# Kernel tuning notes

Measured on AMD Instinct MI355X. Metric: run time of the kernel, lower is better.

Reference implementation:

```python
import jax, jax.numpy as jnp
import numpy as np

H = 2048            # hidden_size
IN = 64             # input_size
EMB = 8             # EMBEDDING_DIMS
LIN = IN - 4 + 4 * EMB  # 92, LSTM input width
NH = 13             # number of prediction heads
MAXO = 9            # max head output width (gear)
HEAD_OUTS = [5, 1, 1, 1, 1, 1, 1, 1, 9, 1, 3, 1, 1]
LN_EPS = 1e-5


def setup_inputs() -> dict:
    key = jax.random.key(0)
    ks = jax.random.split(key, 22)
    s = 1.0 / np.sqrt(H)
    d = {}
    d["lap_cont"] = jax.random.normal(ks[0], (1, 1, IN - 4), jnp.float32)
    d["idx"] = jax.random.randint(ks[1], (1, 1, 4), 0, 5)  # compound, driver, track, team
    d["h_s"] = 0.1 * jax.random.normal(ks[2], (2, 1, H), jnp.float32)
    d["c_s"] = 0.1 * jax.random.normal(ks[3], (2, 1, H), jnp.float32)
    d["emb_team"] = 0.02 * jax.random.normal(ks[4], (10, EMB), jnp.float32)
    d["emb_track"] = 0.02 * jax.random.normal(ks[5], (48, EMB), jnp.float32)
    d["emb_driver"] = 0.02 * jax.random.normal(ks[6], (46, EMB), jnp.float32)
    d["emb_compound"] = 0.02 * jax.random.normal(ks[7], (5, EMB), jnp.float32)
    d["W_ih0"] = s * jax.random.normal(ks[8], (4 * H, LIN), jnp.float32)
    d["W_hh0"] = s * jax.random.normal(ks[9], (4 * H, H), jnp.float32)
    d["b_ih0"] = s * jax.random.normal(ks[10], (4 * H,), jnp.float32)
    d["b_hh0"] = s * jax.random.normal(ks[11], (4 * H,), jnp.float32)
    d["W_ih1"] = s * jax.random.normal(ks[12], (4 * H, H), jnp.float32)
    d["W_hh1"] = s * jax.random.normal(ks[13], (4 * H, H), jnp.float32)
    d["b_ih1"] = s * jax.random.normal(ks[14], (4 * H,), jnp.float32)
    d["b_hh1"] = s * jax.random.normal(ks[15], (4 * H,), jnp.float32)
    d["ln_g"] = jnp.ones((H,), jnp.float32)
    d["ln_b"] = jnp.zeros((H,), jnp.float32)
    d["head_W1"] = 0.02 * jax.random.normal(ks[16], (NH, 64, H), jnp.float32)
    d["head_b1"] = 0.02 * jax.random.normal(ks[17], (NH, 64), jnp.float32)
    d["head_W2"] = 0.02 * jax.random.normal(ks[18], (NH, MAXO, 64), jnp.float32)  # padded to MAXO
    d["head_b2"] = 0.02 * jax.random.normal(ks[19], (NH, MAXO), jnp.float32)
    return d


def _lstm_cell(x, h, c, Wih, Whh, bih, bhh):
    # x:[1,in], h,c:[1,H]; PyTorch gate order i,f,g,o
    g = x @ Wih.T + bih + h @ Whh.T + bhh
    i, f, gg, o = jnp.split(g, 4, axis=-1)
    c_new = jax.nn.sigmoid(f) * c + jax.nn.sigmoid(i) * jnp.tanh(gg)
    h_new = jax.nn.sigmoid(o) * jnp.tanh(c_new)
    return h_new, c_new


def reference(lap_cont, idx, h_s, c_s, emb_team, emb_track, emb_driver, emb_compound,
              W_ih0, W_hh0, b_ih0, b_hh0, W_ih1, W_hh1, b_ih1, b_hh1,
              ln_g, ln_b, head_W1, head_b1, head_W2, head_b2):
    # Embeddings (idx order: compound, driver, track_status, team)
    comp_e = emb_compound[idx[:, :, 0]]
    drv_e = emb_driver[idx[:, :, 1]]
    trk_e = emb_track[idx[:, :, 2]]
    team_e = emb_team[idx[:, :, 3]]
    x = jnp.concatenate([lap_cont, team_e, trk_e, drv_e, comp_e], axis=-1)  # [1,1,LIN]

    x2 = x[0]  # seq_len=1 -> single cell step; [1,LIN]
    h0, c0 = _lstm_cell(x2, h_s[0], c_s[0], W_ih0, W_hh0, b_ih0, b_hh0)
    h1, c1 = _lstm_cell(h0, h_s[1], c_s[1], W_ih1, W_hh1, b_ih1, b_hh1)
    new_h = jnp.stack([h0, h1], axis=0)
    new_c = jnp.stack([c0, c1], axis=0)

    h_t = h1[None]  # [1,1,H]
    mu = jnp.mean(h_t, axis=-1, keepdims=True)
    var = jnp.mean(jnp.square(h_t - mu), axis=-1, keepdims=True)
    h_t = (h_t - mu) * jax.lax.rsqrt(var + LN_EPS) * ln_g + ln_b

    # All 13 heads fused: Dropout is identity at inference
    hid = jax.nn.relu(jnp.einsum('bsh,koh->bsko', h_t, head_W1) + head_b1)  # [1,1,13,64]
    outs = jnp.einsum('bsko,kpo->bskp', hid, head_W2) + head_b2              # [1,1,13,9]

    heads = [outs[:, :, k, :HEAD_OUTS[k]] for k in range(NH)]
    return (new_h, new_c, *heads)
```

## Files before the change

kernel.cpp:

```cpp
#include <hip/hip_runtime.h>

#define H 2048

__device__ __align__(16) float g_p1[4 * H];
__device__ __align__(16) float g_h0[H];
__device__ __align__(16) float g_h1[H];
__device__ __align__(16) float g_hid[13 * 64];

__device__ __forceinline__ float sg(float x) { return 1.f / (1.f + __expf(-x)); }

__device__ __forceinline__ float wred(float x) {
    #pragma unroll
    for (int o = 32; o > 0; o >>= 1) x += __shfl_down(x, o);
    return x;
}

__device__ __forceinline__ float dotg(const float* __restrict__ row,
                                      const float* __restrict__ vec, int lane) {
    float acc = 0.f;
    #pragma unroll
    for (int i = 0; i < 8; i++) {
        int c = i * 256 + lane * 4;
        float4 a = *reinterpret_cast<const float4*>(row + c);
        float4 v = *reinterpret_cast<const float4*>(vec + c);
        acc = fmaf(a.x, v.x, acc); acc = fmaf(a.y, v.y, acc);
        acc = fmaf(a.z, v.z, acc); acc = fmaf(a.w, v.w, acc);
    }
    return acc;
}

__global__ __launch_bounds__(256) void k1(
    const float* __restrict__ lap, const int* __restrict__ idx,
    const float* __restrict__ h_s, const float* __restrict__ c_s,
    const float* __restrict__ e_team, const float* __restrict__ e_trk,
    const float* __restrict__ e_drv, const float* __restrict__ e_cmp,
    const float* __restrict__ Wih0, const float* __restrict__ Whh0,
    const float* __restrict__ bih0, const float* __restrict__ bhh0,
    const float* __restrict__ Whh1, const float* __restrict__ bih1,
    const float* __restrict__ bhh1, float* __restrict__ out)
{
    __shared__ float vec[H];
    __shared__ float xsh[96];
    int tid = threadIdx.x, w = tid >> 6, lane = tid & 63;
    int b = blockIdx.x;
    bool l0 = b < 512;
    const float* src = l0 ? h_s : (h_s + H);
    #pragma unroll
    for (int i = 0; i < 8; i++) vec[tid + i * 256] = src[tid + i * 256];
    if (l0 && tid < 92) {
        float v;
        if (tid < 60)      v = lap[tid];
        else if (tid < 68) v = e_team[idx[3] * 8 + tid - 60];
        else if (tid < 76) v = e_trk [idx[2] * 8 + tid - 68];
        else if (tid < 84) v = e_drv [idx[1] * 8 + tid - 76];
        else               v = e_cmp [idx[0] * 8 + tid - 84];
        xsh[tid] = v;
    }
    __syncthreads();

    if (l0) {
        int j = b * 4 + w;
        float acc[4];
        #pragma unroll
        for (int g = 0; g < 4; g++) {
            long row = j + (long)g * H;
            float a = dotg(Whh0 + row * H, vec, lane);
            const float* wr = Wih0 + row * 92;
            float p = xsh[lane] * wr[lane];
            if (lane < 28) p += xsh[lane + 64] * wr[lane + 64];
            acc[g] = a + p;
        }
        #pragma unroll
        for (int g = 0; g < 4; g++) acc[g] = wred(acc[g]);
        if (lane == 0) {
            float gi = acc[0] + bih0[j]         + bhh0[j];
            float gf = acc[1] + bih0[j + H]     + bhh0[j + H];
            float gg = acc[2] + bih0[j + 2 * H] + bhh0[j + 2 * H];
            float go = acc[3] + bih0[j + 3 * H] + bhh0[j + 3 * H];
            float cp = c_s[j];
            float cn = sg(gf) * cp + sg(gi) * tanhf(gg);
            float hn = sg(go) * tanhf(cn);
            out[j]         = hn;
            out[2 * H + j] = cn;
            g_h0[j] = hn;
        }
    } else {
        int rb = (b - 512) * 16 + w * 4;
        float acc[4];
        #pragma unroll
        for (int r = 0; r < 4; r++) acc[r] = dotg(Whh1 + (long)(rb + r) * H, vec, lane);
        #pragma unroll
        for (int r = 0; r < 4; r++) acc[r] = wred(acc[r]);
        if (lane == 0) {
            #pragma unroll
            for (int r = 0; r < 4; r++) g_p1[rb + r] = acc[r] + bih1[rb + r] + bhh1[rb + r];
        }
    }
}

__global__ __launch_bounds__(256) void k2(
    const float* __restrict__ Wih1, const float* __restrict__ c_s,
    float* __restrict__ out)
{
    __shared__ float vec[H];
    int tid = threadIdx.x, w = tid >> 6, lane = tid & 63;
    #pragma unroll
    for (int i = 0; i < 8; i++) vec[tid + i * 256] = g_h0[tid + i * 256];
    __syncthreads();
    int j = blockIdx.x * 4 + w;
    float acc[4];
    #pragma unroll
    for (int g = 0; g < 4; g++) acc[g] = dotg(Wih1 + (long)(j + g * H) * H, vec, lane);
    #pragma unroll
    for (int g = 0; g < 4; g++) acc[g] = wred(acc[g]);
    if (lane == 0) {
        float gi = acc[0] + g_p1[j];
        float gf = acc[1] + g_p1[j + H];
        float gg = acc[2] + g_p1[j + 2 * H];
        float go = acc[3] + g_p1[j + 3 * H];
        float cp = c_s[H + j];
        float cn = sg(gf) * cp + sg(gi) * tanhf(gg);
        float hn = sg(go) * tanhf(cn);
        out[H + j]     = hn;
        out[3 * H + j] = cn;
        g_h1[j] = hn;
    }
}

__global__ __launch_bounds__(256) void k3(
    const float* __restrict__ ln_g, const float* __restrict__ ln_b,
    const float* __restrict__ W1, const float* __restrict__ b1)
{
    __shared__ float ht[H];
    __shared__ float red[8];
    __shared__ float mvs[2];
    int tid = threadIdx.x, w = tid >> 6, lane = tid & 63;
    float v[8];
    float s = 0.f, s2 = 0.f;
    #pragma unroll
    for (int i = 0; i < 8; i++) {
        float x = g_h1[tid + i * 256];
        v[i] = x; s += x; s2 += x * x;
    }
    s = wred(s); s2 = wred(s2);
    if (lane == 0) { red[w] = s; red[4 + w] = s2; }
    __syncthreads();
    if (tid == 0) {
        float ts = red[0] + red[1] + red[2] + red[3];
        float t2 = red[4] + red[5] + red[6] + red[7];
        float mu = ts / (float)H;
        float var = t2 / (float)H - mu * mu;
        mvs[0] = mu; mvs[1] = rsqrtf(var + 1e-5f);
    }
    __syncthreads();
    float mu = mvs[0], rs = mvs[1];
    #pragma unroll
    for (int i = 0; i < 8; i++) {
        int e = tid + i * 256;
        ht[e] = (v[i] - mu) * rs * ln_g[e] + ln_b[e];
    }
    __syncthreads();
    int k  = blockIdx.x >> 3;
    int u0 = (blockIdx.x & 7) * 8 + w * 2;
    #pragma unroll
    for (int u = 0; u < 2; u++) {
        int o = u0 + u;
        float acc = dotg(W1 + ((long)k * 64 + o) * H, ht, lane);
        acc = wred(acc);
        if (lane == 0) {
            float r = acc + b1[k * 64 + o];
            g_hid[k * 64 + o] = r > 0.f ? r : 0.f;
        }
    }
}

__global__ __launch_bounds__(128) void k4(
    const float* __restrict__ W2, const float* __restrict__ b2,
    float* __restrict__ out)
{
    const int HO[13]  = {5,1,1,1,1,1,1,1,9,1,3,1,1};
    const int OFF[13] = {0,5,6,7,8,9,10,11,12,21,22,25,26};
    int t = threadIdx.x;
    if (t >= 117) return;
    int k = t / 9, p = t % 9;
    if (p >= HO[k]) return;
    const float* wr = W2 + ((long)k * 9 + p) * 64;
    const float* hp = g_hid + k * 64;
    float acc = b2[k * 9 + p];
    #pragma unroll
    for (int o = 0; o < 64; o++) acc = fmaf(hp[o], wr[o], acc);
    out[4 * H + OFF[k] + p] = acc;
}

extern "C" void kernel_launch(void* const* d_in, const int* in_sizes, int n_in,
                              void* d_out, int out_size, void* d_ws, size_t ws_size,
                              hipStream_t stream) {
    const float* lap    = (const float*)d_in[0];
    const int*   idx    = (const int*)  d_in[1];
    const float* h_s    = (const float*)d_in[2];
    const float* c_s    = (const float*)d_in[3];
    const float* e_team = (const float*)d_in[4];
    const float* e_trk  = (const float*)d_in[5];
    const float* e_drv  = (const float*)d_in[6];
    const float* e_cmp  = (const float*)d_in[7];
    const float* Wih0   = (const float*)d_in[8];
    const float* Whh0   = (const float*)d_in[9];
    const float* bih0   = (const float*)d_in[10];
    const float* bhh0   = (const float*)d_in[11];
    const float* Wih1   = (const float*)d_in[12];
    const float* Whh1   = (const float*)d_in[13];
    const float* bih1   = (const float*)d_in[14];
    const float* bhh1   = (const float*)d_in[15];
    const float* ln_g   = (const float*)d_in[16];
    const float* ln_b   = (const float*)d_in[17];
    const float* hW1    = (const float*)d_in[18];
    const float* hb1    = (const float*)d_in[19];
    const float* hW2    = (const float*)d_in[20];
    const float* hb2    = (const float*)d_in[21];
    float* out = (float*)d_out;

    k1<<<1024, 256, 0, stream>>>(lap, idx, h_s, c_s, e_team, e_trk, e_drv, e_cmp,
                                 Wih0, Whh0, bih0, bhh0, Whh1, bih1, bhh1, out);
    k2<<<512, 256, 0, stream>>>(Wih1, c_s, out);
    k3<<<104, 256, 0, stream>>>(ln_g, ln_b, hW1, hb1);
    k4<<<1, 128, 0, stream>>>(hW2, hb2, out);
}
```

Before: 249.8 us.

## Assign one weight row per wave and batch row loads before FMAs

Each wave now computes a single matrix row instead of four, so the GEMV kernels launch four times as many blocks (k3 twice as many). Layer-0 and layer-1 gate combination moves to a shared-memory exchange across the four waves of a block. The dot-product helper issues all eight float4 weight loads up front before the FMA loop, to raise memory-level parallelism. The cost is more blocks that each redundantly stage the hidden vector into LDS, plus an extra block-wide barrier.

```diff
diff --git a/kernel.cpp b/kernel.cpp
--- a/kernel.cpp
+++ b/kernel.cpp
@@ -15,16 +15,18 @@
     return x;
 }
 
-__device__ __forceinline__ float dotg(const float* __restrict__ row,
-                                      const float* __restrict__ vec, int lane) {
+__device__ __forceinline__ float dotrow(const float* __restrict__ row,
+                                        const float* __restrict__ vecLDS, int lane) {
+    float4 a[8];
+    #pragma unroll
+    for (int i = 0; i < 8; i++)
+        a[i] = *reinterpret_cast<const float4*>(row + i * 256 + lane * 4);
     float acc = 0.f;
     #pragma unroll
     for (int i = 0; i < 8; i++) {
-        int c = i * 256 + lane * 4;
-        float4 a = *reinterpret_cast<const float4*>(row + c);
-        float4 v = *reinterpret_cast<const float4*>(vec + c);
-        acc = fmaf(a.x, v.x, acc); acc = fmaf(a.y, v.y, acc);
-        acc = fmaf(a.z, v.z, acc); acc = fmaf(a.w, v.w, acc);
+        float4 v = *reinterpret_cast<const float4*>(vecLDS + i * 256 + lane * 4);
+        acc = fmaf(a[i].x, v.x, acc); acc = fmaf(a[i].y, v.y, acc);
+        acc = fmaf(a[i].z, v.z, acc); acc = fmaf(a[i].w, v.w, acc);
     }
     return acc;
 }
@@ -41,9 +43,10 @@
 {
     __shared__ float vec[H];
     __shared__ float xsh[96];
+    __shared__ float gsh[4];
     int tid = threadIdx.x, w = tid >> 6, lane = tid & 63;
     int b = blockIdx.x;
-    bool l0 = b < 512;
+    bool l0 = b < 2048;
     const float* src = l0 ? h_s : (h_s + H);
     #pragma unroll
     for (int i = 0; i < 8; i++) vec[tid + i * 256] = src[tid + i * 256];
@@ -59,24 +62,17 @@
     __syncthreads();
 
     if (l0) {
-        int j = b * 4 + w;
-        float acc[4];
-        #pragma unroll
-        for (int g = 0; g < 4; g++) {
-            long row = j + (long)g * H;
-            float a = dotg(Whh0 + row * H, vec, lane);
-            const float* wr = Wih0 + row * 92;
-            float p = xsh[lane] * wr[lane];
-            if (lane < 28) p += xsh[lane + 64] * wr[lane + 64];
-            acc[g] = a + p;
-        }
-        #pragma unroll
-        for (int g = 0; g < 4; g++) acc[g] = wred(acc[g]);
-        if (lane == 0) {
-            float gi = acc[0] + bih0[j]         + bhh0[j];
-            float gf = acc[1] + bih0[j + H]     + bhh0[j + H];
-            float gg = acc[2] + bih0[j + 2 * H] + bhh0[j + 2 * H];
-            float go = acc[3] + bih0[j + 3 * H] + bhh0[j + 3 * H];
+        int j = b;
+        long row = j + (long)w * H;
+        float acc = dotrow(Whh0 + row * H, vec, lane);
+        const float* wr = Wih0 + row * 92;
+        float p = xsh[lane] * wr[lane];
+        if (lane < 28) p += xsh[lane + 64] * wr[lane + 64];
+        acc = wred(acc + p);
+        if (lane == 0) gsh[w] = acc + bih0[row] + bhh0[row];
+        __syncthreads();
+        if (tid == 0) {
+            float gi = gsh[0], gf = gsh[1], gg = gsh[2], go = gsh[3];
             float cp = c_s[j];
             float cn = sg(gf) * cp + sg(gi) * tanhf(gg);
             float hn = sg(go) * tanhf(cn);
@@ -85,16 +81,10 @@
             g_h0[j] = hn;
         }
     } else {
-        int rb = (b - 512) * 16 + w * 4;
-        float acc[4];
-        #pragma unroll
-        for (int r = 0; r < 4; r++) acc[r] = dotg(Whh1 + (long)(rb + r) * H, vec, lane);
-        #pragma unroll
-        for (int r = 0; r < 4; r++) acc[r] = wred(acc[r]);
-        if (lane == 0) {
-            #pragma unroll
-            for (int r = 0; r < 4; r++) g_p1[rb + r] = acc[r] + bih1[rb + r] + bhh1[rb + r];
-        }
+        int r = (b - 2048) * 4 + w;
+        float acc = dotrow(Whh1 + (long)r * H, vec, lane);
+        acc = wred(acc);
+        if (lane == 0) g_p1[r] = acc + bih1[r] + bhh1[r];
     }
 }
 
@@ -103,21 +93,19 @@
     float* __restrict__ out)
 {
     __shared__ float vec[H];
+    __shared__ float gsh[4];
     int tid = threadIdx.x, w = tid >> 6, lane = tid & 63;
     #pragma unroll
     for (int i = 0; i < 8; i++) vec[tid + i * 256] = g_h0[tid + i * 256];
     __syncthreads();
-    int j = blockIdx.x * 4 + w;
-    float acc[4];
-    #pragma unroll
-    for (int g = 0; g < 4; g++) acc[g] = dotg(Wih1 + (long)(j + g * H) * H, vec, lane);
-    #pragma unroll
-    for (int g = 0; g < 4; g++) acc[g] = wred(acc[g]);
-    if (lane == 0) {
-        float gi = acc[0] + g_p1[j];
-        float gf = acc[1] + g_p1[j + H];
-        float gg = acc[2] + g_p1[j + 2 * H];
-        float go = acc[3] + g_p1[j + 3 * H];
+    int j = blockIdx.x;
+    long row = j + (long)w * H;
+    float acc = dotrow(Wih1 + row * H, vec, lane);
+    acc = wred(acc);
+    if (lane == 0) gsh[w] = acc + g_p1[row];
+    __syncthreads();
+    if (tid == 0) {
+        float gi = gsh[0], gf = gsh[1], gg = gsh[2], go = gsh[3];
         float cp = c_s[H + j];
         float cn = sg(gf) * cp + sg(gi) * tanhf(gg);
         float hn = sg(go) * tanhf(cn);
@@ -160,17 +148,13 @@
         ht[e] = (v[i] - mu) * rs * ln_g[e] + ln_b[e];
     }
     __syncthreads();
-    int k  = blockIdx.x >> 3;
-    int u0 = (blockIdx.x & 7) * 8 + w * 2;
-    #pragma unroll
-    for (int u = 0; u < 2; u++) {
-        int o = u0 + u;
-        float acc = dotg(W1 + ((long)k * 64 + o) * H, ht, lane);
-        acc = wred(acc);
-        if (lane == 0) {
-            float r = acc + b1[k * 64 + o];
-            g_hid[k * 64 + o] = r > 0.f ? r : 0.f;
-        }
+    int k = blockIdx.x >> 4;
+    int o = (blockIdx.x & 15) * 4 + w;
+    float acc = dotrow(W1 + ((long)k * 64 + o) * H, ht, lane);
+    acc = wred(acc);
+    if (lane == 0) {
+        float r = acc + b1[k * 64 + o];
+        g_hid[k * 64 + o] = r > 0.f ? r : 0.f;
     }
 }
 
@@ -219,9 +203,9 @@
     const float* hb2    = (const float*)d_in[21];
     float* out = (float*)d_out;
 
-    k1<<<1024, 256, 0, stream>>>(lap, idx, h_s, c_s, e_team, e_trk, e_drv, e_cmp,
+    k1<<<4096, 256, 0, stream>>>(lap, idx, h_s, c_s, e_team, e_trk, e_drv, e_cmp,
                                  Wih0, Whh0, bih0, bhh0, Whh1, bih1, bhh1, out);
-    k2<<<512, 256, 0, stream>>>(Wih1, c_s, out);
-    k3<<<104, 256, 0, stream>>>(ln_g, ln_b, hW1, hb1);
+    k2<<<2048, 256, 0, stream>>>(Wih1, c_s, out);
+    k3<<<208, 256, 0, stream>>>(ln_g, ln_b, hW1, hb1);
     k4<<<1, 128, 0, stream>>>(hW2, hb2, out);
 }
```

Result: no change. 247.9 us (-0.8%).
